# Performance work log

Measured on AMD Instinct MI355X. Metric: run time of the kernel, lower is better.

The kernel has to match this reference:

```python
import jax, jax.numpy as jnp
import numpy as np

B, S, D, H, DFF, V, LAT, L = 64, 256, 512, 8, 2048, 128, 512, 6
MAXLEN = 256
NEG = -1e9
EPS = 1e-5


def setup_inputs() -> dict:
    key = jax.random.key(0)
    ks = jax.random.split(key, 32)
    s = 0.02
    rn = lambda k, shape: jax.random.normal(k, shape, jnp.float32) * s
    inp = {
        "z": jax.random.normal(ks[0], (B, LAT), jnp.float32),
        "tgt_seq": jax.random.randint(ks[1], (B, S), 0, V),
        "emb": rn(ks[2], (V, D)).at[0].set(0.0),  # padding_idx=0 row zeroed
        "pos": rn(ks[3], (MAXLEN, D)),
        "proj_w": rn(ks[4], (D, LAT)),
        "proj_b": jnp.zeros((D,), jnp.float32),
        "sa_w": rn(ks[5], (L, 3 * D, D)),
        "sa_b": jnp.zeros((L, 3 * D), jnp.float32),
        "sa_ow": rn(ks[6], (L, D, D)),
        "sa_ob": jnp.zeros((L, D), jnp.float32),
        "ca_w": rn(ks[7], (L, 3 * D, D)),
        "ca_b": jnp.zeros((L, 3 * D), jnp.float32),
        "ca_ow": rn(ks[8], (L, D, D)),
        "ca_ob": jnp.zeros((L, D), jnp.float32),
        "ln1_s": jnp.ones((L, D), jnp.float32),
        "ln1_b": jnp.zeros((L, D), jnp.float32),
        "ln2_s": jnp.ones((L, D), jnp.float32),
        "ln2_b": jnp.zeros((L, D), jnp.float32),
        "ln3_s": jnp.ones((L, D), jnp.float32),
        "ln3_b": jnp.zeros((L, D), jnp.float32),
        "ff1_w": rn(ks[9], (L, DFF, D)),
        "ff1_b": jnp.zeros((L, DFF), jnp.float32),
        "ff2_w": rn(ks[10], (L, D, DFF)),
        "ff2_b": jnp.zeros((L, D), jnp.float32),
        "fc_w": rn(ks[11], (V, D)),
        "fc_b": jnp.zeros((V,), jnp.float32),
    }
    return inp


def _ln(x, s, b):
    m = jnp.mean(x, -1, keepdims=True)
    v = jnp.mean(jnp.square(x - m), -1, keepdims=True)
    return (x - m) * jax.lax.rsqrt(v + EPS) * s + b


def _mha(q_in, k_in, v_in, w, b, ow, ob, mask=None):
    # torch MultiheadAttention: packed in_proj [3D, D], out_proj [D, D]
    wq, wk, wv = w[:D], w[D:2 * D], w[2 * D:]
    bq, bk, bv = b[:D], b[D:2 * D], b[2 * D:]
    dh = D // H
    split = lambda t: t.reshape(t.shape[0], t.shape[1], H, dh)
    q = split(q_in @ wq.T + bq)  # [B,Sq,H,dh]
    k = split(k_in @ wk.T + bk)  # [B,Sk,H,dh]
    v = split(v_in @ wv.T + bv)
    scores = jnp.einsum("bqhd,bkhd->bhqk", q, k) / np.sqrt(dh).astype(np.float32)
    if mask is not None:
        scores = scores + mask
    attn = jax.nn.softmax(scores, axis=-1)
    out = jnp.einsum("bhqk,bkhd->bqhd", attn, v).reshape(q_in.shape[0], q_in.shape[1], D)
    return out @ ow.T + ob


def reference(z, tgt_seq, emb, pos, proj_w, proj_b, sa_w, sa_b, sa_ow, sa_ob,
              ca_w, ca_b, ca_ow, ca_ob, ln1_s, ln1_b, ln2_s, ln2_b, ln3_s, ln3_b,
              ff1_w, ff1_b, ff2_w, ff2_b, fc_w, fc_b):
    # memory = proj(z), length-1 cross-attention memory: [B,1,D]
    mem = (z @ proj_w.T + proj_b)[:, None, :]
    seq_len = tgt_seq.shape[1]
    x = emb[tgt_seq] + pos[:seq_len][None]  # [B,S,D]
    causal = jnp.where(jnp.tril(jnp.ones((seq_len, seq_len), bool)), 0.0, NEG)
    for i in range(L):  # post-norm TransformerDecoderLayer (torch default)
        sa = _mha(x, x, x, sa_w[i], sa_b[i], sa_ow[i], sa_ob[i], causal)
        x = _ln(x + sa, ln1_s[i], ln1_b[i])
        ca = _mha(x, mem, mem, ca_w[i], ca_b[i], ca_ow[i], ca_ob[i])
        x = _ln(x + ca, ln2_s[i], ln2_b[i])
        ff = jax.nn.relu(x @ ff1_w[i].T + ff1_b[i]) @ ff2_w[i].T + ff2_b[i]
        x = _ln(x + ff, ln3_s[i], ln3_b[i])
    logits = x @ fc_w.T + fc_b  # [B,S,V]
    return logits
```

## Files before the change

kernel.cpp:

```cpp
#include <hip/hip_runtime.h>

typedef unsigned int uint;
typedef unsigned short ushort;

typedef __attribute__((ext_vector_type(8))) __bf16 bf16x8;
typedef __attribute__((ext_vector_type(4))) float f32x4;

#define B_ 64
#define S_ 256
#define D_ 512
#define H_ 8
#define DFF_ 2048
#define V_ 128
#define L_ 6
#define BS_ (B_ * S_)

__device__ __forceinline__ float blo(uint u) { return __uint_as_float(u << 16); }
__device__ __forceinline__ float bhi(uint u) { return __uint_as_float(u & 0xffff0000u); }
__device__ __forceinline__ float b2f(ushort u) { return __uint_as_float(((uint)u) << 16); }
__device__ __forceinline__ ushort f2b(float f) {
  uint u = __float_as_uint(f);
  return (ushort)((u + 0x7fffu + ((u >> 16) & 1u)) >> 16);
}
__device__ __forceinline__ uint pack2(float a, float b) {
  return (uint)f2b(a) | ((uint)f2b(b) << 16);
}

#define GLOAD16(gp, lp)                                                        \
  __builtin_amdgcn_global_load_lds(                                            \
      (const __attribute__((address_space(1))) void*)(gp),                     \
      (__attribute__((address_space(3))) void*)(lp), 16, 0, 0)

__global__ __launch_bounds__(256) void conv_kernel(const float* __restrict__ src,
                                                   ushort* __restrict__ dst) {
  size_t p = (size_t)blockIdx.x * 256 + threadIdx.x;
  float2 v = ((const float2*)src)[p];
  ((uint*)dst)[p] = pack2(v.x, v.y);
}

__global__ __launch_bounds__(256) void embed_kernel(
    const int* __restrict__ tgt, const float* __restrict__ emb,
    const float* __restrict__ pos, ushort* __restrict__ x16) {
  int p = blockIdx.x * 256 + threadIdx.x;
  int row = p >> 8;
  int d2 = p & 255;
  int s = row & (S_ - 1);
  int tok = tgt[row];
  float2 e = ((const float2*)emb)[tok * 256 + d2];
  float2 pp = ((const float2*)pos)[s * 256 + d2];
  ((uint*)x16)[p] = pack2(e.x + pp.x, e.y + pp.y);
}

template <int MODE>
__global__ __launch_bounds__(256) void gemm_rs(
    const ushort* __restrict__ A, const ushort* __restrict__ W,
    const float* __restrict__ bias, void* __restrict__ Cv, int N, int K,
    int As, int Ws, int Cs) {
  __shared__ ushort la[2][8192];
  __shared__ ushort lb[2][8192];
  const int tid = threadIdx.x;
  const int wv = tid >> 6, lane = tid & 63;

  const int nwg = gridDim.x * gridDim.y;
  int lid = blockIdx.x + gridDim.x * blockIdx.y;
  lid = (lid & 7) * (nwg >> 3) + (lid >> 3);
  const int bx = lid % gridDim.x;
  const int by = lid / gridDim.x;
  const int m0 = by << 7, n0 = bx << 7;

  const int wm = (wv >> 1) << 6, wn = (wv & 1) << 6;
  const int tr = lane & 15, tq = lane >> 4;

  const int lin0 = wv * 1024 + lane * 8;
  const int am0 = lin0 >> 5, ac0 = lin0 & 31;
  const int lin1 = lin0 + 512;
  const int am1 = lin1 >> 5, ac1 = lin1 & 31;

  const ushort* pa0 = A + (size_t)(m0 + am0) * As + ac0;
  const ushort* pa1 = A + (size_t)(m0 + am1) * As + ac1;
  const ushort* pb0 = W + (size_t)(n0 + am0) * Ws + ac0;
  const ushort* pb1 = W + (size_t)(n0 + am1) * Ws + ac1;

  f32x4 acc[4][4];
#pragma unroll
  for (int i = 0; i < 4; ++i)
#pragma unroll
    for (int j = 0; j < 4; ++j) acc[i][j] = (f32x4)(0.f);

  const int KT = K >> 6;
  uint4 ra0, ra1, ra2, ra3, rb0, rb1, rb2, rb3;

#define LOADR(t)                                                               \
  do {                                                                         \
    const int kb_ = (t) << 6;                                                  \
    ra0 = *(const uint4*)(pa0 + kb_);                                          \
    ra1 = *(const uint4*)(pa1 + kb_);                                          \
    ra2 = *(const uint4*)(pa0 + kb_ + 32);                                     \
    ra3 = *(const uint4*)(pa1 + kb_ + 32);                                     \
    rb0 = *(const uint4*)(pb0 + kb_);                                          \
    rb1 = *(const uint4*)(pb1 + kb_);                                          \
    rb2 = *(const uint4*)(pb0 + kb_ + 32);                                     \
    rb3 = *(const uint4*)(pb1 + kb_ + 32);                                     \
  } while (0)
#define WRITR(d)                                                               \
  do {                                                                         \
    *(uint4*)&la[d][lin0] = ra0;                                               \
    *(uint4*)&la[d][lin1] = ra1;                                               \
    *(uint4*)&la[d][4096 + lin0] = ra2;                                        \
    *(uint4*)&la[d][4096 + lin1] = ra3;                                        \
    *(uint4*)&lb[d][lin0] = rb0;                                               \
    *(uint4*)&lb[d][lin1] = rb1;                                               \
    *(uint4*)&lb[d][4096 + lin0] = rb2;                                        \
    *(uint4*)&lb[d][4096 + lin1] = rb3;                                        \
  } while (0)

  LOADR(0);
  WRITR(0);
  __syncthreads();

  for (int t = 0; t < KT; ++t) {
    const int d = t & 1;
    if (t + 1 < KT) LOADR(t + 1);
    bf16x8 av[2][4], bv[2][4];
#pragma unroll
    for (int s = 0; s < 2; ++s) {
#pragma unroll
      for (int i = 0; i < 4; ++i)
        av[s][i] =
            *(const bf16x8*)&la[d][s * 4096 + (wm + i * 16 + tr) * 32 + tq * 8];
#pragma unroll
      for (int j = 0; j < 4; ++j)
        bv[s][j] =
            *(const bf16x8*)&lb[d][s * 4096 + (wn + j * 16 + tr) * 32 + tq * 8];
    }
#pragma unroll
    for (int s = 0; s < 2; ++s)
#pragma unroll
      for (int i = 0; i < 4; ++i)
#pragma unroll
        for (int j = 0; j < 4; ++j)
          acc[i][j] = __builtin_amdgcn_mfma_f32_16x16x32_bf16(
              av[s][i], bv[s][j], acc[i][j], 0, 0, 0);
    if (t + 1 < KT) WRITR(d ^ 1);
    __syncthreads();
  }
#undef LOADR
#undef WRITR

#pragma unroll
  for (int j = 0; j < 4; ++j) {
    const int gn = n0 + wn + j * 16 + tr;
    float bj = 0.f;
    if (MODE != 2) bj = bias[gn];
    float scl = 1.f;
    if (MODE == 4) scl = (gn < 512) ? 0.18033688011112042f : 1.f;
#pragma unroll
    for (int i = 0; i < 4; ++i) {
      const int gmb = m0 + wm + i * 16 + tq * 4;
#pragma unroll
      for (int r = 0; r < 4; ++r) {
        const size_t idx = (size_t)(gmb + r) * Cs + gn;
        float v = acc[i][j][r] + bj;
        if (MODE == 1) v = fmaxf(v, 0.f);
        if (MODE == 4) v *= scl;
        if (MODE == 2) {
          ushort* C = (ushort*)Cv;
          C[idx] = f2b(b2f(C[idx]) + acc[i][j][r]);
        } else
          ((ushort*)Cv)[idx] = f2b(v);
      }
    }
  }
}

template <int MODE>
__global__ __launch_bounds__(256) void gemm_bt(
    const ushort* __restrict__ A, const ushort* __restrict__ W,
    const float* __restrict__ bias, void* __restrict__ Cv, int N, int K,
    int As, int Ws, int Cs) {
  __shared__ ushort la[128 * 32];
  __shared__ ushort lb[128 * 32];
  const int tid = threadIdx.x;
  const int wv = tid >> 6, lane = tid & 63;

  const int nwg = gridDim.x * gridDim.y;
  int lid = blockIdx.x + gridDim.x * blockIdx.y;
  lid = (lid & 7) * (nwg >> 3) + (lid >> 3);
  const int bx = lid % gridDim.x;
  const int by = lid / gridDim.x;
  const int m0 = by << 7, n0 = bx << 7;

  const int wm = (wv >> 1) << 6, wn = (wv & 1) << 6;
  const int tr = lane & 15, tq = lane >> 4;

  const int lin0 = wv * 1024 + lane * 8;
  const int lin1 = lin0 + 512;
  const int am0 = lin0 >> 5, ac0 = lin0 & 31;
  const int am1 = lin1 >> 5, ac1 = lin1 & 31;

  const ushort* pa0 = A + (size_t)(m0 + am0) * As + ac0;
  const ushort* pa1 = A + (size_t)(m0 + am1) * As + ac1;
  const ushort* pb0 = W + (size_t)(n0 + am0) * Ws + ac0;
  const ushort* pb1 = W + (size_t)(n0 + am1) * Ws + ac1;
  ushort* la0 = &la[wv * 1024];
  ushort* la1 = &la[wv * 1024 + 512];
  ushort* lb0 = &lb[wv * 1024];
  ushort* lb1 = &lb[wv * 1024 + 512];

  f32x4 acc[4][4];
#pragma unroll
  for (int i = 0; i < 4; ++i)
#pragma unroll
    for (int j = 0; j < 4; ++j) acc[i][j] = (f32x4)(0.f);

  const int KT = K >> 5;
  for (int kt = 0; kt < KT; ++kt) {
    const int kb = kt << 5;
    GLOAD16(pa0 + kb, la0);
    GLOAD16(pa1 + kb, la1);
    GLOAD16(pb0 + kb, lb0);
    GLOAD16(pb1 + kb, lb1);
    __syncthreads();
    bf16x8 av[4], bv[4];
#pragma unroll
    for (int i = 0; i < 4; ++i)
      av[i] = *(const bf16x8*)&la[(wm + i * 16 + tr) * 32 + tq * 8];
#pragma unroll
    for (int j = 0; j < 4; ++j)
      bv[j] = *(const bf16x8*)&lb[(wn + j * 16 + tr) * 32 + tq * 8];
#pragma unroll
    for (int i = 0; i < 4; ++i)
#pragma unroll
      for (int j = 0; j < 4; ++j)
        acc[i][j] =
            __builtin_amdgcn_mfma_f32_16x16x32_bf16(av[i], bv[j], acc[i][j], 0, 0, 0);
    __syncthreads();
  }

#pragma unroll
  for (int j = 0; j < 4; ++j) {
    const int gn = n0 + wn + j * 16 + tr;
    float bj = 0.f;
    if (MODE != 2) bj = bias[gn];
    float scl = 1.f;
    if (MODE == 4) scl = (gn < 512) ? 0.18033688011112042f : 1.f;
#pragma unroll
    for (int i = 0; i < 4; ++i) {
      const int gmb = m0 + wm + i * 16 + tq * 4;
#pragma unroll
      for (int r = 0; r < 4; ++r) {
        const size_t idx = (size_t)(gmb + r) * Cs + gn;
        float v = acc[i][j][r] + bj;
        if (MODE == 1) v = fmaxf(v, 0.f);
        if (MODE == 4) v *= scl;
        if (MODE == 3)
          ((float*)Cv)[idx] = v;
        else if (MODE == 2) {
          ushort* C = (ushort*)Cv;
          C[idx] = f2b(b2f(C[idx]) + acc[i][j][r]);
        } else
          ((ushort*)Cv)[idx] = f2b(v);
      }
    }
  }
}

__global__ __launch_bounds__(256) void gemm_btf(
    const ushort* __restrict__ A0, long zA, const float* __restrict__ W0,
    long zW, const float* __restrict__ bias0, long zb, ushort* __restrict__ C0,
    long zC, int N, int K, int As, int Ws, int Cs) {
  const int zz = blockIdx.z;
  const ushort* A = A0 + zA * zz;
  const float* W = W0 + zW * zz;
  const float* bias = bias0 + zb * zz;
  ushort* C = C0 + zC * zz;

  __shared__ ushort la[128 * 32];
  __shared__ ushort lb[128 * 32];
  const int tid = threadIdx.x;
  const int wv = tid >> 6, lane = tid & 63;
  const int m0 = blockIdx.y << 7, n0 = blockIdx.x << 7;
  const int wm = (wv >> 1) << 6, wn = (wv & 1) << 6;
  const int tr = lane & 15, tq = lane >> 4;

  const int lin0 = wv * 1024 + lane * 8;
  const int lin1 = lin0 + 512;
  const int am0 = lin0 >> 5, ac0 = lin0 & 31;
  const int am1 = lin1 >> 5, ac1 = lin1 & 31;

  const ushort* pa0 = A + (size_t)(m0 + am0) * As + ac0;
  const ushort* pa1 = A + (size_t)(m0 + am1) * As + ac1;
  const float* pb0 = W + (size_t)(n0 + am0) * Ws + ac0;
  const float* pb1 = W + (size_t)(n0 + am1) * Ws + ac1;

  f32x4 acc[4][4];
#pragma unroll
  for (int i = 0; i < 4; ++i)
#pragma unroll
    for (int j = 0; j < 4; ++j) acc[i][j] = (f32x4)(0.f);

  const int KT = K >> 5;
  for (int kt = 0; kt < KT; ++kt) {
    const int kb = kt << 5;
    uint4 ra0 = *(const uint4*)(pa0 + kb);
    uint4 ra1 = *(const uint4*)(pa1 + kb);
    float4 f00 = *(const float4*)(pb0 + kb);
    float4 f01 = *(const float4*)(pb0 + kb + 4);
    float4 f10 = *(const float4*)(pb1 + kb);
    float4 f11 = *(const float4*)(pb1 + kb + 4);
    uint4 rb0 = make_uint4(pack2(f00.x, f00.y), pack2(f00.z, f00.w),
                           pack2(f01.x, f01.y), pack2(f01.z, f01.w));
    uint4 rb1 = make_uint4(pack2(f10.x, f10.y), pack2(f10.z, f10.w),
                           pack2(f11.x, f11.y), pack2(f11.z, f11.w));
    __syncthreads();
    *(uint4*)&la[lin0] = ra0;
    *(uint4*)&la[lin1] = ra1;
    *(uint4*)&lb[lin0] = rb0;
    *(uint4*)&lb[lin1] = rb1;
    __syncthreads();
    bf16x8 av[4], bv[4];
#pragma unroll
    for (int i = 0; i < 4; ++i)
      av[i] = *(const bf16x8*)&la[(wm + i * 16 + tr) * 32 + tq * 8];
#pragma unroll
    for (int j = 0; j < 4; ++j)
      bv[j] = *(const bf16x8*)&lb[(wn + j * 16 + tr) * 32 + tq * 8];
#pragma unroll
    for (int i = 0; i < 4; ++i)
#pragma unroll
      for (int j = 0; j < 4; ++j)
        acc[i][j] =
            __builtin_amdgcn_mfma_f32_16x16x32_bf16(av[i], bv[j], acc[i][j], 0, 0, 0);
  }

#pragma unroll
  for (int j = 0; j < 4; ++j) {
    const int gn = n0 + wn + j * 16 + tr;
    const float bj = bias[gn];
#pragma unroll
    for (int i = 0; i < 4; ++i) {
      const int gmb = m0 + wm + i * 16 + tq * 4;
#pragma unroll
      for (int r = 0; r < 4; ++r)
        C[(size_t)(gmb + r) * Cs + gn] = f2b(acc[i][j][r] + bj);
    }
  }
}

__global__ __launch_bounds__(128) void attn_mfma(ushort* __restrict__ qkv) {
  __shared__ ushort lk[64 * 72];
  __shared__ ushort lvT[64 * 72];
  __shared__ ushort lp[2 * 64 * 72];
  const int qp = blockIdx.x, h = blockIdx.y, b = blockIdx.z;
  const int tid = threadIdx.x;
  const int g = tid >> 6, lane = tid & 63;
  const int tr = lane & 15, tq = lane >> 4;
  const int qc = qp * 2 + g;
  const int q0 = qc << 6;
  ushort* myp = &lp[g * 64 * 72];

  bf16x8 qf[4][2];
#pragma unroll
  for (int i = 0; i < 4; ++i)
#pragma unroll
    for (int s = 0; s < 2; ++s)
      qf[i][s] = *(const bf16x8*)(qkv +
                                  (size_t)(b * 256 + q0 + i * 16 + tr) * 1536 +
                                  h * 64 + s * 32 + tq * 8);

  f32x4 o[4][4];
  float pl[4][4];
#pragma unroll
  for (int i = 0; i < 4; ++i)
#pragma unroll
    for (int j = 0; j < 4; ++j) {
      o[i][j] = (f32x4)(0.f);
      pl[i][j] = 0.f;
    }

  const int key = tid >> 1, half = tid & 1;
  const int cmax = qp * 2 + 1;
  for (int c = 0; c <= cmax; ++c) {
    __syncthreads();
    const ushort* gk =
        qkv + (size_t)(b * 256 + c * 64 + key) * 1536 + 512 + h * 64 + half * 32;
#pragma unroll
    for (int u = 0; u < 4; ++u)
      *(uint4*)&lk[key * 72 + half * 32 + u * 8] = *(const uint4*)(gk + u * 8);
    ushort vloc[32];
#pragma unroll
    for (int u = 0; u < 4; ++u)
      *(uint4*)&vloc[u * 8] = *(const uint4*)(gk + 512 + u * 8);
#pragma unroll
    for (int dd = 0; dd < 32; ++dd)
      lvT[(half * 32 + dd) * 72 + key] = vloc[dd];
    __syncthreads();

    if (c <= qc) {
      f32x4 Sv[4][4];
#pragma unroll
      for (int i = 0; i < 4; ++i)
#pragma unroll
        for (int j = 0; j < 4; ++j) Sv[i][j] = (f32x4)(0.f);
      bf16x8 kf[4][2];
#pragma unroll
      for (int j = 0; j < 4; ++j)
#pragma unroll
        for (int s = 0; s < 2; ++s)
          kf[j][s] = *(const bf16x8*)&lk[(j * 16 + tr) * 72 + s * 32 + tq * 8];
#pragma unroll
      for (int i = 0; i < 4; ++i)
#pragma unroll
        for (int j = 0; j < 4; ++j) {
          Sv[i][j] = __builtin_amdgcn_mfma_f32_16x16x32_bf16(qf[i][0], kf[j][0],
                                                             Sv[i][j], 0, 0, 0);
          Sv[i][j] = __builtin_amdgcn_mfma_f32_16x16x32_bf16(qf[i][1], kf[j][1],
                                                             Sv[i][j], 0, 0, 0);
        }
      const bool diag = (c == qc);
#pragma unroll
      for (int i = 0; i < 4; ++i)
#pragma unroll
        for (int j = 0; j < 4; ++j)
#pragma unroll
          for (int r = 0; r < 4; ++r) {
            float e = exp2f(Sv[i][j][r]);
            if (diag && (j * 16 + tr) > (i * 16 + tq * 4 + r)) e = 0.f;
            pl[i][r] += e;
            myp[(i * 16 + tq * 4 + r) * 72 + j * 16 + tr] =
                (ushort)(__float_as_uint(e) >> 16);
          }
#pragma unroll
      for (int s = 0; s < 2; ++s) {
        bf16x8 vf[4], af[4];
#pragma unroll
        for (int jn = 0; jn < 4; ++jn)
          vf[jn] = *(const bf16x8*)&lvT[(jn * 16 + tr) * 72 + s * 32 + tq * 8];
#pragma unroll
        for (int im = 0; im < 4; ++im)
          af[im] = *(const bf16x8*)&myp[(im * 16 + tr) * 72 + s * 32 + tq * 8];
#pragma unroll
        for (int im = 0; im < 4; ++im)
#pragma unroll
          for (int jn = 0; jn < 4; ++jn)
            o[im][jn] = __builtin_amdgcn_mfma_f32_16x16x32_bf16(af[im], vf[jn],
                                                                o[im][jn], 0, 0, 0);
      }
    }
  }

#pragma unroll
  for (int i = 0; i < 4; ++i)
#pragma unroll
    for (int r = 0; r < 4; ++r) {
      float v = pl[i][r];
      v += __shfl_xor(v, 1, 64);
      v += __shfl_xor(v, 2, 64);
      v += __shfl_xor(v, 4, 64);
      v += __shfl_xor(v, 8, 64);
      pl[i][r] = 1.f / v;
    }

#pragma unroll
  for (int i = 0; i < 4; ++i)
#pragma unroll
    for (int j = 0; j < 4; ++j)
#pragma unroll
      for (int r = 0; r < 4; ++r)
        qkv[(size_t)(b * 256 + q0 + i * 16 + tq * 4 + r) * 1536 + h * 64 +
            j * 16 + tr] = f2b(o[i][j][r] * pl[i][r]);
}

__global__ __launch_bounds__(256) void ln12_kernel(
    ushort* __restrict__ x16, const uint* __restrict__ d1,
    const uint* __restrict__ cavec, const float* __restrict__ s1,
    const float* __restrict__ b1, const float* __restrict__ s2,
    const float* __restrict__ b2p) {
  const int r = blockIdx.x, t = threadIdx.x;
  const int lane = t & 63, wv = t >> 6;
  uint* xr = (uint*)x16 + (size_t)r * 256;
  uint xu = xr[t];
  uint du = d1[(size_t)r * 768 + t];
  float v0 = blo(xu) + blo(du), v1 = bhi(xu) + bhi(du);
  __shared__ float redA[4][2], redB[4][2];
  float sm = v0 + v1, sq = v0 * v0 + v1 * v1;
#pragma unroll
  for (int o = 32; o > 0; o >>= 1) {
    sm += __shfl_xor(sm, o, 64);
    sq += __shfl_xor(sq, o, 64);
  }
  if (lane == 0) {
    redA[wv][0] = sm;
    redA[wv][1] = sq;
  }
  __syncthreads();
  sm = redA[0][0] + redA[1][0] + redA[2][0] + redA[3][0];
  sq = redA[0][1] + redA[1][1] + redA[2][1] + redA[3][1];
  float mean = sm * (1.f / 512.f);
  float var = sq * (1.f / 512.f) - mean * mean;
  float rs = rsqrtf(var + 1e-5f);
  float2 sa = ((const float2*)s1)[t];
  float2 ba = ((const float2*)b1)[t];
  uint cu = cavec[(size_t)(r >> 8) * 256 + t];
  float w0 = (v0 - mean) * rs * sa.x + ba.x + blo(cu);
  float w1 = (v1 - mean) * rs * sa.y + ba.y + bhi(cu);
  sm = w0 + w1;
  sq = w0 * w0 + w1 * w1;
#pragma unroll
  for (int o = 32; o > 0; o >>= 1) {
    sm += __shfl_xor(sm, o, 64);
    sq += __shfl_xor(sq, o, 64);
  }
  if (lane == 0) {
    redB[wv][0] = sm;
    redB[wv][1] = sq;
  }
  __syncthreads();
  sm = redB[0][0] + redB[1][0] + redB[2][0] + redB[3][0];
  sq = redB[0][1] + redB[1][1] + redB[2][1] + redB[3][1];
  mean = sm * (1.f / 512.f);
  var = sq * (1.f / 512.f) - mean * mean;
  rs = rsqrtf(var + 1e-5f);
  float2 sb = ((const float2*)s2)[t];
  float2 bb = ((const float2*)b2p)[t];
  float y0 = (w0 - mean) * rs * sb.x + bb.x;
  float y1 = (w1 - mean) * rs * sb.y + bb.y;
  xr[t] = pack2(y0, y1);
}

__global__ __launch_bounds__(256) void ln_kernel(
    ushort* __restrict__ x16, const uint* __restrict__ delta, int DsU,
    const float* __restrict__ sc, const float* __restrict__ bi) {
  const int r = blockIdx.x, t = threadIdx.x;
  const int lane = t & 63, wv = t >> 6;
  uint* xr = (uint*)x16 + (size_t)r * 256;
  uint xu = xr[t];
  uint du = delta[(size_t)r * DsU + t];
  float v0 = blo(xu) + blo(du), v1 = bhi(xu) + bhi(du);
  float sm = v0 + v1, sq = v0 * v0 + v1 * v1;
#pragma unroll
  for (int o = 32; o > 0; o >>= 1) {
    sm += __shfl_xor(sm, o, 64);
    sq += __shfl_xor(sq, o, 64);
  }
  __shared__ float red[4][2];
  if (lane == 0) {
    red[wv][0] = sm;
    red[wv][1] = sq;
  }
  __syncthreads();
  sm = red[0][0] + red[1][0] + red[2][0] + red[3][0];
  sq = red[0][1] + red[1][1] + red[2][1] + red[3][1];
  float mean = sm * (1.f / 512.f);
  float var = sq * (1.f / 512.f) - mean * mean;
  float rs = rsqrtf(var + 1e-5f);
  float2 s2 = ((const float2*)sc)[t];
  float2 b2 = ((const float2*)bi)[t];
  float y0 = (v0 - mean) * rs * s2.x + b2.x;
  float y1 = (v1 - mean) * rs * s2.y + b2.y;
  xr[t] = pack2(y0, y1);
}

extern "C" void kernel_launch(void* const* d_in, const int* in_sizes, int n_in,
                              void* d_out, int out_size, void* d_ws,
                              size_t ws_size, hipStream_t stream) {
  (void)in_sizes; (void)n_in; (void)out_size; (void)ws_size;
  const float* z = (const float*)d_in[0];
  const int* tgt = (const int*)d_in[1];
  const float* emb = (const float*)d_in[2];
  const float* pos = (const float*)d_in[3];
  const float* projw = (const float*)d_in[4];
  const float* projb = (const float*)d_in[5];
  const float* saw = (const float*)d_in[6];
  const float* sab = (const float*)d_in[7];
  const float* saow = (const float*)d_in[8];
  const float* saob = (const float*)d_in[9];
  const float* caw = (const float*)d_in[10];
  const float* cab = (const float*)d_in[11];
  const float* caow = (const float*)d_in[12];
  const float* caob = (const float*)d_in[13];
  const float* ln1s = (const float*)d_in[14];
  const float* ln1b = (const float*)d_in[15];
  const float* ln2s = (const float*)d_in[16];
  const float* ln2b = (const float*)d_in[17];
  const float* ln3s = (const float*)d_in[18];
  const float* ln3b = (const float*)d_in[19];
  const float* ff1w = (const float*)d_in[20];
  const float* ff1b = (const float*)d_in[21];
  const float* ff2w = (const float*)d_in[22];
  const float* ff2b = (const float*)d_in[23];
  const float* fcw = (const float*)d_in[24];
  const float* fcb = (const float*)d_in[25];

  char* w8 = (char*)d_ws;
  ushort* x16 = (ushort*)w8;
  ushort* qkv = (ushort*)(w8 + (16u << 20));
  ushort* hbuf = qkv;
  ushort* fdel = (ushort*)(w8 + (48u << 20));
  ushort* z16 = (ushort*)(w8 + (64u << 20));
  ushort* memv16 = z16 + 128 * 512;
  ushort* cav16 = memv16 + 128 * 512;
  ushort* cavec16 = cav16 + (size_t)L_ * 128 * 512;
  ushort* wsaw = (ushort*)(w8 + (66u << 20));
  ushort* wsaow = wsaw + (size_t)L_ * 1536 * 512;
  ushort* wff1 = wsaow + (size_t)L_ * 512 * 512;
  ushort* wff2 = wff1 + (size_t)L_ * 2048 * 512;
  ushort* wfcw = wff2 + (size_t)L_ * 512 * 2048;

  conv_kernel<<<(L_ * 1536 * 512) / 512, 256, 0, stream>>>(saw, wsaw);
  conv_kernel<<<(L_ * 512 * 512) / 512, 256, 0, stream>>>(saow, wsaow);
  conv_kernel<<<(L_ * 2048 * 512) / 512, 256, 0, stream>>>(ff1w, wff1);
  conv_kernel<<<(L_ * 512 * 2048) / 512, 256, 0, stream>>>(ff2w, wff2);
  conv_kernel<<<(V_ * 512) / 512, 256, 0, stream>>>(fcw, wfcw);
  conv_kernel<<<(B_ * 512) / 512, 256, 0, stream>>>(z, z16);

  embed_kernel<<<16384, 256, 0, stream>>>(tgt, emb, pos, x16);

  gemm_btf<<<dim3(4, 1, 1), 256, 0, stream>>>(z16, 0, projw, 0, projb, 0,
                                              memv16, 0, 512, 512, 512, 512, 512);
  gemm_btf<<<dim3(4, 1, L_), 256, 0, stream>>>(
      memv16, 0, caw + 1024 * 512, (long)1536 * 512, cab + 1024, 1536, cav16,
      (long)128 * 512, 512, 512, 512, 512, 512);
  gemm_btf<<<dim3(4, 1, L_), 256, 0, stream>>>(
      cav16, (long)128 * 512, caow, (long)512 * 512, caob, 512, cavec16,
      (long)128 * 512, 512, 512, 512, 512, 512);

  for (int i = 0; i < L_; ++i) {
    gemm_rs<4><<<dim3(12, 128), 256, 0, stream>>>(
        x16, wsaw + (size_t)i * 1536 * 512, sab + i * 1536, qkv, 1536, 512, 512,
        512, 1536);
    attn_mfma<<<dim3(2, H_, B_), 128, 0, stream>>>(qkv);
    gemm_rs<0><<<dim3(4, 128), 256, 0, stream>>>(
        qkv, wsaow + (size_t)i * 512 * 512, saob + i * 512, qkv + 512, 512, 512,
        1536, 512, 1536);
    ln12_kernel<<<16384, 256, 0, stream>>>(
        x16, (const uint*)(qkv + 512), (const uint*)(cavec16 + (size_t)i * 128 * 512),
        ln1s + i * 512, ln1b + i * 512, ln2s + i * 512, ln2b + i * 512);
    gemm_rs<1><<<dim3(8, 128), 256, 0, stream>>>(
        x16, wff1 + (size_t)i * 2048 * 512, ff1b + i * 2048, hbuf, 1024, 512,
        512, 512, 1024);
    gemm_rs<0><<<dim3(4, 128), 256, 0, stream>>>(
        hbuf, wff2 + (size_t)i * 512 * 2048, ff2b + i * 512, fdel, 512, 1024,
        1024, 2048, 512);
    gemm_rs<1><<<dim3(8, 128), 256, 0, stream>>>(
        x16, wff1 + ((size_t)i * 2048 + 1024) * 512, ff1b + i * 2048 + 1024,
        hbuf, 1024, 512, 512, 512, 1024);
    gemm_rs<2><<<dim3(4, 128), 256, 0, stream>>>(
        hbuf, wff2 + (size_t)i * 512 * 2048 + 1024, (const float*)0, fdel, 512,
        1024, 1024, 2048, 512);
    ln_kernel<<<16384, 256, 0, stream>>>(x16, (const uint*)fdel, 256,
                                         ln3s + i * 512, ln3b + i * 512);
  }
  gemm_bt<3><<<dim3(1, 128), 256, 0, stream>>>(x16, wfcw, fcb, d_out, 128, 512,
                                               512, 512, 128);
}
```

Before: 1.612 ms.

## Stage gemm_rs epilogue through LDS for vectorized stores, double-register prefetch

Restructures the register-staged GEMM. The K loop is unrolled by two, with two register sets so each global prefetch is issued a full tile earlier. The MFMA operands are swapped so each lane holds four consecutive output columns. The epilogue now writes bf16 results into padded LDS and then stores 16-byte rows with coalesced writes, including a vectorized read-add-write path for the residual mode. This replaces the scattered 2-byte global stores, at the cost of more registers and an extra LDS pass and barrier. One side effect: the residual mode now rounds the GEMM result to bf16 before adding it.

After: 1.611 ms. No clear change (-0.0%).

```diff
diff --git a/kernel.cpp b/kernel.cpp
--- a/kernel.cpp
+++ b/kernel.cpp
@@ -51,13 +51,37 @@
   ((uint*)x16)[p] = pack2(e.x + pp.x, e.y + pp.y);
 }
 
+__device__ __forceinline__ void compute_tile(const ushort* base, int wm, int wn,
+                                             int tr, int tq,
+                                             f32x4 (&acc)[4][4]) {
+  const ushort* sA = base;
+  const ushort* sB = base + 8192;
+  bf16x8 av[2][4], bv[2][4];
+#pragma unroll
+  for (int s = 0; s < 2; ++s) {
+#pragma unroll
+    for (int i = 0; i < 4; ++i)
+      av[s][i] = *(const bf16x8*)&sA[s * 4096 + (wm + i * 16 + tr) * 32 + tq * 8];
+#pragma unroll
+    for (int j = 0; j < 4; ++j)
+      bv[s][j] = *(const bf16x8*)&sB[s * 4096 + (wn + j * 16 + tr) * 32 + tq * 8];
+  }
+#pragma unroll
+  for (int s = 0; s < 2; ++s)
+#pragma unroll
+    for (int i = 0; i < 4; ++i)
+#pragma unroll
+      for (int j = 0; j < 4; ++j)
+        acc[i][j] = __builtin_amdgcn_mfma_f32_16x16x32_bf16(bv[s][j], av[s][i],
+                                                            acc[i][j], 0, 0, 0);
+}
+
 template <int MODE>
 __global__ __launch_bounds__(256) void gemm_rs(
     const ushort* __restrict__ A, const ushort* __restrict__ W,
     const float* __restrict__ bias, void* __restrict__ Cv, int N, int K,
     int As, int Ws, int Cs) {
-  __shared__ ushort la[2][8192];
-  __shared__ ushort lb[2][8192];
+  __shared__ ushort lsh[32768];
   const int tid = threadIdx.x;
   const int wv = tid >> 6, lane = tid & 63;
 
@@ -88,88 +112,119 @@
     for (int j = 0; j < 4; ++j) acc[i][j] = (f32x4)(0.f);
 
   const int KT = K >> 6;
-  uint4 ra0, ra1, ra2, ra3, rb0, rb1, rb2, rb3;
-
-#define LOADR(t)                                                               \
+
+  uint4 sa0, sa1, sa2, sa3, sb0, sb1, sb2, sb3;
+  uint4 ta0, ta1, ta2, ta3, tb0, tb1, tb2, tb3;
+
+#define LOADS(t)                                                               \
   do {                                                                         \
     const int kb_ = (t) << 6;                                                  \
-    ra0 = *(const uint4*)(pa0 + kb_);                                          \
-    ra1 = *(const uint4*)(pa1 + kb_);                                          \
-    ra2 = *(const uint4*)(pa0 + kb_ + 32);                                     \
-    ra3 = *(const uint4*)(pa1 + kb_ + 32);                                     \
-    rb0 = *(const uint4*)(pb0 + kb_);                                          \
-    rb1 = *(const uint4*)(pb1 + kb_);                                          \
-    rb2 = *(const uint4*)(pb0 + kb_ + 32);                                     \
-    rb3 = *(const uint4*)(pb1 + kb_ + 32);                                     \
+    sa0 = *(const uint4*)(pa0 + kb_);                                          \
+    sa1 = *(const uint4*)(pa1 + kb_);                                          \
+    sa2 = *(const uint4*)(pa0 + kb_ + 32);                                     \
+    sa3 = *(const uint4*)(pa1 + kb_ + 32);                                     \
+    sb0 = *(const uint4*)(pb0 + kb_);                                          \
+    sb1 = *(const uint4*)(pb1 + kb_);                                          \
+    sb2 = *(const uint4*)(pb0 + kb_ + 32);                                     \
+    sb3 = *(const uint4*)(pb1 + kb_ + 32);                                     \
   } while (0)
-#define WRITR(d)                                                               \
+#define LOADT(t)                                                               \
   do {                                                                         \
-    *(uint4*)&la[d][lin0] = ra0;                                               \
-    *(uint4*)&la[d][lin1] = ra1;                                               \
-    *(uint4*)&la[d][4096 + lin0] = ra2;                                        \
-    *(uint4*)&la[d][4096 + lin1] = ra3;                                        \
-    *(uint4*)&lb[d][lin0] = rb0;                                               \
-    *(uint4*)&lb[d][lin1] = rb1;                                               \
-    *(uint4*)&lb[d][4096 + lin0] = rb2;                                        \
-    *(uint4*)&lb[d][4096 + lin1] = rb3;                                        \
+    const int kb_ = (t) << 6;                                                  \
+    ta0 = *(const uint4*)(pa0 + kb_);                                          \
+    ta1 = *(const uint4*)(pa1 + kb_);                                          \
+    ta2 = *(const uint4*)(pa0 + kb_ + 32);                                     \
+    ta3 = *(const uint4*)(pa1 + kb_ + 32);                                     \
+    tb0 = *(const uint4*)(pb0 + kb_);                                          \
+    tb1 = *(const uint4*)(pb1 + kb_);                                          \
+    tb2 = *(const uint4*)(pb0 + kb_ + 32);                                     \
+    tb3 = *(const uint4*)(pb1 + kb_ + 32);                                     \
   } while (0)
-
-  LOADR(0);
-  WRITR(0);
+#define WRITS(d)                                                               \
+  do {                                                                         \
+    ushort* b_ = lsh + (d) * 16384;                                            \
+    *(uint4*)&b_[lin0] = sa0;                                                  \
+    *(uint4*)&b_[lin1] = sa1;                                                  \
+    *(uint4*)&b_[4096 + lin0] = sa2;                                           \
+    *(uint4*)&b_[4096 + lin1] = sa3;                                           \
+    *(uint4*)&b_[8192 + lin0] = sb0;                                           \
+    *(uint4*)&b_[8192 + lin1] = sb1;                                           \
+    *(uint4*)&b_[12288 + lin0] = sb2;                                          \
+    *(uint4*)&b_[12288 + lin1] = sb3;                                          \
+  } while (0)
+#define WRITT(d)                                                               \
+  do {                                                                         \
+    ushort* b_ = lsh + (d) * 16384;                                            \
+    *(uint4*)&b_[lin0] = ta0;                                                  \
+    *(uint4*)&b_[lin1] = ta1;                                                  \
+    *(uint4*)&b_[4096 + lin0] = ta2;                                           \
+    *(uint4*)&b_[4096 + lin1] = ta3;                                           \
+    *(uint4*)&b_[8192 + lin0] = tb0;                                           \
+    *(uint4*)&b_[8192 + lin1] = tb1;                                           \
+    *(uint4*)&b_[12288 + lin0] = tb2;                                          \
+    *(uint4*)&b_[12288 + lin1] = tb3;                                          \
+  } while (0)
+
+  LOADS(0);
+  LOADT(1);
+  WRITS(0);
   __syncthreads();
 
-  for (int t = 0; t < KT; ++t) {
-    const int d = t & 1;
-    if (t + 1 < KT) LOADR(t + 1);
-    bf16x8 av[2][4], bv[2][4];
-#pragma unroll
-    for (int s = 0; s < 2; ++s) {
-#pragma unroll
-      for (int i = 0; i < 4; ++i)
-        av[s][i] =
-            *(const bf16x8*)&la[d][s * 4096 + (wm + i * 16 + tr) * 32 + tq * 8];
-#pragma unroll
-      for (int j = 0; j < 4; ++j)
-        bv[s][j] =
-            *(const bf16x8*)&lb[d][s * 4096 + (wn + j * 16 + tr) * 32 + tq * 8];
+  for (int t = 0; t < KT; t += 2) {
+    if (t + 2 < KT) LOADS(t + 2);
+    compute_tile(lsh, wm, wn, tr, tq, acc);
+    if (t + 1 < KT) WRITT(1);
+    __syncthreads();
+    if (t + 3 < KT) LOADT(t + 3);
+    compute_tile(lsh + 16384, wm, wn, tr, tq, acc);
+    if (t + 2 < KT) WRITS(0);
+    __syncthreads();
+  }
+#undef LOADS
+#undef LOADT
+#undef WRITS
+#undef WRITT
+
+#pragma unroll
+  for (int i = 0; i < 4; ++i)
+#pragma unroll
+    for (int j = 0; j < 4; ++j) {
+      const int gn4 = n0 + wn + j * 16 + tq * 4;
+      float b0 = 0.f, b1 = 0.f, b2 = 0.f, b3 = 0.f;
+      if (MODE != 2) {
+        float4 bb = ((const float4*)bias)[gn4 >> 2];
+        b0 = bb.x; b1 = bb.y; b2 = bb.z; b3 = bb.w;
+      }
+      float v0 = acc[i][j][0] + b0, v1 = acc[i][j][1] + b1,
+            v2 = acc[i][j][2] + b2, v3 = acc[i][j][3] + b3;
+      if (MODE == 1) {
+        v0 = fmaxf(v0, 0.f); v1 = fmaxf(v1, 0.f);
+        v2 = fmaxf(v2, 0.f); v3 = fmaxf(v3, 0.f);
+      }
+      if (MODE == 4) {
+        const float scl = (gn4 < 512) ? 0.18033688011112042f : 1.f;
+        v0 *= scl; v1 *= scl; v2 *= scl; v3 *= scl;
+      }
+      uint2 pk;
+      pk.x = pack2(v0, v1);
+      pk.y = pack2(v2, v3);
+      *(uint2*)&lsh[(wm + i * 16 + tr) * 136 + wn + j * 16 + tq * 4] = pk;
     }
-#pragma unroll
-    for (int s = 0; s < 2; ++s)
-#pragma unroll
-      for (int i = 0; i < 4; ++i)
-#pragma unroll
-        for (int j = 0; j < 4; ++j)
-          acc[i][j] = __builtin_amdgcn_mfma_f32_16x16x32_bf16(
-              av[s][i], bv[s][j], acc[i][j], 0, 0, 0);
-    if (t + 1 < KT) WRITR(d ^ 1);
-    __syncthreads();
-  }
-#undef LOADR
-#undef WRITR
-
-#pragma unroll
-  for (int j = 0; j < 4; ++j) {
-    const int gn = n0 + wn + j * 16 + tr;
-    float bj = 0.f;
-    if (MODE != 2) bj = bias[gn];
-    float scl = 1.f;
-    if (MODE == 4) scl = (gn < 512) ? 0.18033688011112042f : 1.f;
-#pragma unroll
-    for (int i = 0; i < 4; ++i) {
-      const int gmb = m0 + wm + i * 16 + tq * 4;
-#pragma unroll
-      for (int r = 0; r < 4; ++r) {
-        const size_t idx = (size_t)(gmb + r) * Cs + gn;
-        float v = acc[i][j][r] + bj;
-        if (MODE == 1) v = fmaxf(v, 0.f);
-        if (MODE == 4) v *= scl;
-        if (MODE == 2) {
-          ushort* C = (ushort*)Cv;
-          C[idx] = f2b(b2f(C[idx]) + acc[i][j][r]);
-        } else
-          ((ushort*)Cv)[idx] = f2b(v);
-      }
+  __syncthreads();
+#pragma unroll
+  for (int u = 0; u < 8; ++u) {
+    const int f = u * 256 + tid;
+    const int row = f >> 4, sl = f & 15;
+    uint4 val = *(const uint4*)&lsh[row * 136 + sl * 8];
+    ushort* gp = (ushort*)Cv + (size_t)(m0 + row) * Cs + n0 + sl * 8;
+    if (MODE == 2) {
+      uint4 c = *(const uint4*)gp;
+      val.x = pack2(blo(val.x) + blo(c.x), bhi(val.x) + bhi(c.x));
+      val.y = pack2(blo(val.y) + blo(c.y), bhi(val.y) + bhi(c.y));
+      val.z = pack2(blo(val.z) + blo(c.z), bhi(val.z) + bhi(c.z));
+      val.w = pack2(blo(val.w) + blo(c.w), bhi(val.w) + bhi(c.w));
     }
+    *(uint4*)gp = val;
   }
 }
 
```

## Widen gemm_rs tile to 128x256 with K-step 32 and merged LDS buffer

Applied to the files above, without the earlier changes.

The register-staged GEMM now computes a 128x256 output tile per workgroup instead of 128x128. Each wave accumulates a 64x128 sub-tile, which gives more MFMA work per A fragment load. The K-step per iteration drops from 64 to 32, which keeps the LDS footprint similar in a single merged buffer, and all launch grids are halved along N. This aims to raise arithmetic intensity and cut global and LDS traffic per FLOP. The cost is twice as many accumulator registers, which may lower occupancy, plus twice as many loop iterations and barriers, and fewer workgroups per GEMM.

After: 1.904 ms. +18.1%, slower.

```diff
diff --git a/kernel.cpp b/kernel.cpp
--- a/kernel.cpp
+++ b/kernel.cpp
@@ -56,8 +56,7 @@
     const ushort* __restrict__ A, const ushort* __restrict__ W,
     const float* __restrict__ bias, void* __restrict__ Cv, int N, int K,
     int As, int Ws, int Cs) {
-  __shared__ ushort la[2][8192];
-  __shared__ ushort lb[2][8192];
+  __shared__ ushort lsh[2][12288];
   const int tid = threadIdx.x;
   const int wv = tid >> 6, lane = tid & 63;
 
@@ -66,9 +65,10 @@
   lid = (lid & 7) * (nwg >> 3) + (lid >> 3);
   const int bx = lid % gridDim.x;
   const int by = lid / gridDim.x;
-  const int m0 = by << 7, n0 = bx << 7;
-
-  const int wm = (wv >> 1) << 6, wn = (wv & 1) << 6;
+  const int m0 = by << 7, n0 = bx << 8;
+
+  const int wm = (wv >> 1) << 6;
+  const int wn = (wv & 1) << 7;
   const int tr = lane & 15, tq = lane >> 4;
 
   const int lin0 = wv * 1024 + lane * 8;
@@ -80,38 +80,37 @@
   const ushort* pa1 = A + (size_t)(m0 + am1) * As + ac1;
   const ushort* pb0 = W + (size_t)(n0 + am0) * Ws + ac0;
   const ushort* pb1 = W + (size_t)(n0 + am1) * Ws + ac1;
-
-  f32x4 acc[4][4];
+  const ushort* pb2 = W + (size_t)(n0 + 128 + am0) * Ws + ac0;
+  const ushort* pb3 = W + (size_t)(n0 + 128 + am1) * Ws + ac1;
+
+  f32x4 acc[4][8];
 #pragma unroll
   for (int i = 0; i < 4; ++i)
 #pragma unroll
-    for (int j = 0; j < 4; ++j) acc[i][j] = (f32x4)(0.f);
-
-  const int KT = K >> 6;
-  uint4 ra0, ra1, ra2, ra3, rb0, rb1, rb2, rb3;
+    for (int j = 0; j < 8; ++j) acc[i][j] = (f32x4)(0.f);
+
+  const int KT = K >> 5;
+
+  uint4 ra0, ra1, rb0, rb1, rb2, rb3;
 
 #define LOADR(t)                                                               \
   do {                                                                         \
-    const int kb_ = (t) << 6;                                                  \
+    const int kb_ = (t) << 5;                                                  \
     ra0 = *(const uint4*)(pa0 + kb_);                                          \
     ra1 = *(const uint4*)(pa1 + kb_);                                          \
-    ra2 = *(const uint4*)(pa0 + kb_ + 32);                                     \
-    ra3 = *(const uint4*)(pa1 + kb_ + 32);                                     \
     rb0 = *(const uint4*)(pb0 + kb_);                                          \
     rb1 = *(const uint4*)(pb1 + kb_);                                          \
-    rb2 = *(const uint4*)(pb0 + kb_ + 32);                                     \
-    rb3 = *(const uint4*)(pb1 + kb_ + 32);                                     \
+    rb2 = *(const uint4*)(pb2 + kb_);                                          \
+    rb3 = *(const uint4*)(pb3 + kb_);                                          \
   } while (0)
 #define WRITR(d)                                                               \
   do {                                                                         \
-    *(uint4*)&la[d][lin0] = ra0;                                               \
-    *(uint4*)&la[d][lin1] = ra1;                                               \
-    *(uint4*)&la[d][4096 + lin0] = ra2;                                        \
-    *(uint4*)&la[d][4096 + lin1] = ra3;                                        \
-    *(uint4*)&lb[d][lin0] = rb0;                                               \
-    *(uint4*)&lb[d][lin1] = rb1;                                               \
-    *(uint4*)&lb[d][4096 + lin0] = rb2;                                        \
-    *(uint4*)&lb[d][4096 + lin1] = rb3;                                        \
+    *(uint4*)&lsh[d][lin0] = ra0;                                              \
+    *(uint4*)&lsh[d][lin1] = ra1;                                              \
+    *(uint4*)&lsh[d][4096 + lin0] = rb0;                                       \
+    *(uint4*)&lsh[d][4096 + lin1] = rb1;                                       \
+    *(uint4*)&lsh[d][8192 + lin0] = rb2;                                       \
+    *(uint4*)&lsh[d][8192 + lin1] = rb3;                                       \
   } while (0)
 
   LOADR(0);
@@ -121,26 +120,19 @@
   for (int t = 0; t < KT; ++t) {
     const int d = t & 1;
     if (t + 1 < KT) LOADR(t + 1);
-    bf16x8 av[2][4], bv[2][4];
-#pragma unroll
-    for (int s = 0; s < 2; ++s) {
-#pragma unroll
-      for (int i = 0; i < 4; ++i)
-        av[s][i] =
-            *(const bf16x8*)&la[d][s * 4096 + (wm + i * 16 + tr) * 32 + tq * 8];
-#pragma unroll
-      for (int j = 0; j < 4; ++j)
-        bv[s][j] =
-            *(const bf16x8*)&lb[d][s * 4096 + (wn + j * 16 + tr) * 32 + tq * 8];
-    }
-#pragma unroll
-    for (int s = 0; s < 2; ++s)
-#pragma unroll
-      for (int i = 0; i < 4; ++i)
-#pragma unroll
-        for (int j = 0; j < 4; ++j)
-          acc[i][j] = __builtin_amdgcn_mfma_f32_16x16x32_bf16(
-              av[s][i], bv[s][j], acc[i][j], 0, 0, 0);
+    bf16x8 av[4], bv[8];
+#pragma unroll
+    for (int i = 0; i < 4; ++i)
+      av[i] = *(const bf16x8*)&lsh[d][(wm + i * 16 + tr) * 32 + tq * 8];
+#pragma unroll
+    for (int j = 0; j < 8; ++j)
+      bv[j] = *(const bf16x8*)&lsh[d][4096 + (wn + j * 16 + tr) * 32 + tq * 8];
+#pragma unroll
+    for (int i = 0; i < 4; ++i)
+#pragma unroll
+      for (int j = 0; j < 8; ++j)
+        acc[i][j] = __builtin_amdgcn_mfma_f32_16x16x32_bf16(av[i], bv[j],
+                                                            acc[i][j], 0, 0, 0);
     if (t + 1 < KT) WRITR(d ^ 1);
     __syncthreads();
   }
@@ -148,7 +140,7 @@
 #undef WRITR
 
 #pragma unroll
-  for (int j = 0; j < 4; ++j) {
+  for (int j = 0; j < 8; ++j) {
     const int gn = n0 + wn + j * 16 + tr;
     float bj = 0.f;
     if (MODE != 2) bj = bias[gn];
@@ -626,26 +618,26 @@
       (long)128 * 512, 512, 512, 512, 512, 512);
 
   for (int i = 0; i < L_; ++i) {
-    gemm_rs<4><<<dim3(12, 128), 256, 0, stream>>>(
+    gemm_rs<4><<<dim3(6, 128), 256, 0, stream>>>(
         x16, wsaw + (size_t)i * 1536 * 512, sab + i * 1536, qkv, 1536, 512, 512,
         512, 1536);
     attn_mfma<<<dim3(2, H_, B_), 128, 0, stream>>>(qkv);
-    gemm_rs<0><<<dim3(4, 128), 256, 0, stream>>>(
+    gemm_rs<0><<<dim3(2, 128), 256, 0, stream>>>(
         qkv, wsaow + (size_t)i * 512 * 512, saob + i * 512, qkv + 512, 512, 512,
         1536, 512, 1536);
     ln12_kernel<<<16384, 256, 0, stream>>>(
         x16, (const uint*)(qkv + 512), (const uint*)(cavec16 + (size_t)i * 128 * 512),
         ln1s + i * 512, ln1b + i * 512, ln2s + i * 512, ln2b + i * 512);
-    gemm_rs<1><<<dim3(8, 128), 256, 0, stream>>>(
+    gemm_rs<1><<<dim3(4, 128), 256, 0, stream>>>(
         x16, wff1 + (size_t)i * 2048 * 512, ff1b + i * 2048, hbuf, 1024, 512,
         512, 512, 1024);
-    gemm_rs<0><<<dim3(4, 128), 256, 0, stream>>>(
+    gemm_rs<0><<<dim3(2, 128), 256, 0, stream>>>(
         hbuf, wff2 + (size_t)i * 512 * 2048, ff2b + i * 512, fdel, 512, 1024,
         1024, 2048, 512);
-    gemm_rs<1><<<dim3(8, 128), 256, 0, stream>>>(
+    gemm_rs<1><<<dim3(4, 128), 256, 0, stream>>>(
         x16, wff1 + ((size_t)i * 2048 + 1024) * 512, ff1b + i * 2048 + 1024,
         hbuf, 1024, 512, 512, 512, 1024);
-    gemm_rs<2><<<dim3(4, 128), 256, 0, stream>>>(
+    gemm_rs<2><<<dim3(2, 128), 256, 0, stream>>>(
         hbuf, wff2 + (size_t)i * 512 * 2048 + 1024, (const float*)0, fdel, 512,
         1024, 1024, 2048, 512);
     ln_kernel<<<16384, 256, 0, stream>>>(x16, (const uint*)fdel, 256,
```
